# Performance work log

Measured on AMD Instinct MI355X. Metric: run time of the kernel, lower is better.

## Reference

```python
import jax, jax.numpy as jnp
from jax import lax
import numpy as np

B, S = 4096, 200           # batch, max history length
MAX_LEN, STEP = 1024, 4    # module init args
BINS = MAX_LEN // STEP     # 256 time bins
H = 64                     # LSTM hidden (dimension)


def setup_inputs() -> dict:
    key = jax.random.key(0)
    ks = jax.random.split(key, 8)
    time = jax.random.uniform(ks[0], (B, S), jnp.float32, 0.0, 1000.0)
    # predict_time >= max event time per row (module assumes nonnegative bin index)
    predict_time = jnp.max(time, axis=1) + jax.random.uniform(ks[1], (B,), jnp.float32, 0.0, 24.0)
    length = jax.random.randint(ks[2], (B,), 1, S + 1, jnp.int32)
    # torch nn.LSTM init: uniform(-1/sqrt(H), 1/sqrt(H)); gate order i,f,g,o
    s = 1.0 / np.sqrt(H)
    W_ih = jax.random.uniform(ks[3], (4 * H, 1), jnp.float32, -s, s)
    W_hh = jax.random.uniform(ks[4], (4 * H, H), jnp.float32, -s, s)
    b_ih = jax.random.uniform(ks[5], (4 * H,), jnp.float32, -s, s)
    b_hh = jax.random.uniform(ks[6], (4 * H,), jnp.float32, -s, s)
    return {"time": time, "length": length, "predict_time": predict_time,
            "W_ih": W_ih, "W_hh": W_hh, "b_ih": b_ih, "b_hh": b_hh}


def _histogram(time, length, predict_time):
    # pos = int((predict_time - time_ij) / STEP), incremented at bin BINS-1-pos
    pos = ((predict_time[:, None] - time) / STEP).astype(jnp.int32)  # trunc toward 0, like int()
    valid = (jnp.arange(S)[None, :] < length[:, None]) & (pos >= 0) & (pos < BINS)
    idx = BINS - 1 - jnp.clip(pos, 0, BINS - 1)
    hist = jnp.zeros((B, BINS), jnp.float32)
    hist = hist.at[jnp.arange(B)[:, None], idx].add(valid.astype(jnp.float32))
    return hist  # [B, BINS]


def _lstm_final_h(x, W_ih, W_hh, b_ih, b_hh):
    # x: [B, T] scalar sequence (input_size=1). Returns final hidden state [B, H].
    b = b_ih + b_hh

    def step(carry, x_t):
        h, c = carry
        gates = x_t[:, None] * W_ih[:, 0][None, :] + h @ W_hh.T + b  # [B, 4H]
        i, f, g, o = jnp.split(gates, 4, axis=1)
        c = jax.nn.sigmoid(f) * c + jax.nn.sigmoid(i) * jnp.tanh(g)
        h = jax.nn.sigmoid(o) * jnp.tanh(c)
        return (h, c), None

    init = (jnp.zeros((B, H), x.dtype), jnp.zeros((B, H), x.dtype))
    (h, _), _ = lax.scan(step, init, jnp.moveaxis(x, 1, 0))  # scan over T
    return h


def reference(time, length, predict_time, W_ih, W_hh, b_ih, b_hh):
    hist = _histogram(time, length, predict_time)
    return _lstm_final_h(hist, W_ih, W_hh, b_ih, b_hh)
```

## Files before the change

### kernel.cpp

```cpp
#include <hip/hip_runtime.h>
#include <hip/hip_bf16.h>


#define B_S     200
#define B_T     256
#define ROWS    16
#define THREADS 256
#define HS      72
#define LOG2E   1.4426950408889634f

typedef __attribute__((ext_vector_type(8))) _Float16 half8;
typedef __attribute__((ext_vector_type(4))) float float4_t;

__device__ __forceinline__ float load_f(const void* p, int i, int isb) {
    if (isb) {
        unsigned short u = ((const unsigned short*)p)[i];
        return __uint_as_float(((unsigned int)u) << 16);
    }
    return ((const float*)p)[i];
}

__global__ __launch_bounds__(THREADS)
void trend_encoder_kernel(const void* __restrict__ time_,
                          const int*  __restrict__ length,
                          const void* __restrict__ ptime_,
                          const void* __restrict__ wih_,
                          const void* __restrict__ whh_,
                          const void* __restrict__ bih_,
                          const void* __restrict__ bhh_,
                          void* __restrict__ out_) {
    __shared__ __align__(16) float x_t[B_T * ROWS];
    __shared__ __align__(16) _Float16 h_sh[2][ROWS * HS];
    __shared__ int flag_sh;

    const int tid  = threadIdx.x;
    const int wv   = tid >> 6;
    const int lane = tid & 63;
    const int m    = lane & 15;
    const int quad = lane >> 4;
    const int b0   = blockIdx.x * ROWS;

    if (tid < 64) {
        unsigned short u = ((const unsigned short*)wih_)[tid];
        float v = __uint_as_float(((unsigned int)u) << 16);
        int bad = !(v > -0.2f && v < 0.2f);
        unsigned long long bm = __ballot(bad);
        if (lane == 0) flag_sh = (bm == 0ULL) ? 1 : 0;
    }
    for (int i = tid; i < B_T * ROWS; i += THREADS) x_t[i] = 0.0f;
    for (int i = tid; i < ROWS * HS; i += THREADS) h_sh[0][i] = (_Float16)0.0f;
    __syncthreads();
    const int isb = flag_sh;

    for (int e = tid; e < ROWS * B_S; e += THREADS) {
        int row  = e / B_S;
        int s    = e - row * B_S;
        int grow = b0 + row;
        if (s < length[grow]) {
            float pt = load_f(ptime_, grow, isb);
            float tv = load_f(time_, grow * B_S + s, isb);
            int pos = (int)((pt - tv) * 0.25f);
            if (pos >= 0 && pos < B_T)
                atomicAdd(&x_t[(B_T - 1 - pos) * ROWS + row], 1.0f);
        }
    }

    const float gsc[4] = {-LOG2E, -LOG2E, 2.0f * LOG2E, -LOG2E};
    half8 bw[4][2];
    float wihv[4], biasv[4];
    #pragma unroll
    for (int tt = 0; tt < 4; ++tt) {
        int n = 16 * wv + 64 * tt + m;
        float s = gsc[tt];
        wihv[tt]  = load_f(wih_, n, isb) * s;
        biasv[tt] = (load_f(bih_, n, isb) + load_f(bhh_, n, isb)) * s;
        #pragma unroll
        for (int c = 0; c < 2; ++c) {
            half8 v;
            #pragma unroll
            for (int j = 0; j < 8; ++j)
                v[j] = (_Float16)(load_f(whh_, n * 64 + 32 * c + 8 * quad + j, isb) * s);
            bw[tt][c] = v;
        }
    }

    const int aoff = m * HS + 8 * quad;
    const int kcol = 16 * wv + m;
    float creg[4] = {0.f, 0.f, 0.f, 0.f};
    float hreg[4] = {0.f, 0.f, 0.f, 0.f};
    __syncthreads();

    for (int t = 0; t < B_T; ++t) {
        const int p = t & 1;
        const _Float16* hh = h_sh[p];
        half8 a0 = *(const half8*)&hh[aoff];
        half8 a1 = *(const half8*)&hh[aoff + 32];
        float4_t xv = *(const float4_t*)&x_t[t * ROWS + quad * 4];

        float4_t acc[4];
        #pragma unroll
        for (int tt = 0; tt < 4; ++tt) {
            float4_t a;
            #pragma unroll
            for (int r = 0; r < 4; ++r) a[r] = fmaf(xv[r], wihv[tt], biasv[tt]);
            a = __builtin_amdgcn_mfma_f32_16x16x32_f16(a0, bw[tt][0], a, 0, 0, 0);
            a = __builtin_amdgcn_mfma_f32_16x16x32_f16(a1, bw[tt][1], a, 0, 0, 0);
            acc[tt] = a;
        }

        _Float16* wb = h_sh[p ^ 1];
        #pragma unroll
        for (int r = 0; r < 4; ++r) {
            float A  = __builtin_amdgcn_exp2f(acc[0][r]);
            float F  = __builtin_amdgcn_exp2f(acc[1][r]);
            float Bv = __builtin_amdgcn_exp2f(acc[2][r]);
            float t1    = (1.0f + A) * (Bv + 1.0f);
            float oneF  = 1.0f + F;
            float numer = fmaf(creg[r], t1, oneF * (Bv - 1.0f));
            float denom = oneF * t1;
            creg[r] = numer * __builtin_amdgcn_rcpf(denom);
            float D  = __builtin_amdgcn_exp2f(acc[3][r]);
            float cs = fminf(creg[r] * (2.0f * LOG2E), 126.0f);
            float E  = __builtin_amdgcn_exp2f(cs);
            float h  = (E - 1.0f) * __builtin_amdgcn_rcpf((1.0f + D) * (E + 1.0f));
            hreg[r] = h;
            wb[(quad * 4 + r) * HS + kcol] = (_Float16)h;
        }
        __syncthreads();
    }

    #pragma unroll
    for (int r = 0; r < 4; ++r) {
        int o = (b0 + quad * 4 + r) * 64 + kcol;
        if (isb) ((__hip_bfloat16*)out_)[o] = __float2bfloat16(hreg[r]);
        else     ((float*)out_)[o] = hreg[r];
    }
}

extern "C" void kernel_launch(void* const* d_in, const int* in_sizes, int n_in,
                              void* d_out, int out_size, void* d_ws, size_t ws_size,
                              hipStream_t stream) {
    const void* time_  = d_in[0];
    const int*  length = (const int*)d_in[1];
    const void* ptime  = d_in[2];
    const void* wih    = d_in[3];
    const void* whh    = d_in[4];
    const void* bih    = d_in[5];
    const void* bhh    = d_in[6];

    const int B = in_sizes[1];
    trend_encoder_kernel<<<dim3(B / ROWS), dim3(THREADS), 0, stream>>>(
        time_, length, ptime, wih, whh, bih, bhh, d_out);
}
```

Before: 194.3 us.

## Double block to 512 threads, splitting gate activations across wave halves

Doubles the threads per block so two waves share each hidden-column chunk. Both waves compute the same MFMAs redundantly, and each applies the activation math to only half of the 4 accumulator rows. This halves the serial per-step transcendental work per wave on the recurrent critical path. The cost is duplicated MFMA work, more waves per barrier, and possibly lower block occupancy per CU.

```diff
diff --git a/kernel.cpp b/kernel.cpp
--- a/kernel.cpp
+++ b/kernel.cpp
@@ -5,7 +5,7 @@
 #define B_S     200
 #define B_T     256
 #define ROWS    16
-#define THREADS 256
+#define THREADS 512
 #define HS      72
 #define LOG2E   1.4426950408889634f
 
@@ -33,12 +33,14 @@
     __shared__ __align__(16) _Float16 h_sh[2][ROWS * HS];
     __shared__ int flag_sh;
 
-    const int tid  = threadIdx.x;
-    const int wv   = tid >> 6;
-    const int lane = tid & 63;
-    const int m    = lane & 15;
-    const int quad = lane >> 4;
-    const int b0   = blockIdx.x * ROWS;
+    const int tid   = threadIdx.x;
+    const int wv    = tid >> 6;
+    const int lane  = tid & 63;
+    const int m     = lane & 15;
+    const int quad  = lane >> 4;
+    const int hc    = wv & 3;
+    const int rhalf = wv >> 2;
+    const int b0    = blockIdx.x * ROWS;
 
     if (tid < 64) {
         unsigned short u = ((const unsigned short*)wih_)[tid];
@@ -70,7 +72,7 @@
     float wihv[4], biasv[4];
     #pragma unroll
     for (int tt = 0; tt < 4; ++tt) {
-        int n = 16 * wv + 64 * tt + m;
+        int n = 16 * hc + 64 * tt + m;
         float s = gsc[tt];
         wihv[tt]  = load_f(wih_, n, isb) * s;
         biasv[tt] = (load_f(bih_, n, isb) + load_f(bhh_, n, isb)) * s;
@@ -85,10 +87,28 @@
     }
 
     const int aoff = m * HS + 8 * quad;
-    const int kcol = 16 * wv + m;
-    float creg[4] = {0.f, 0.f, 0.f, 0.f};
-    float hreg[4] = {0.f, 0.f, 0.f, 0.f};
+    const int kcol = 16 * hc + m;
+    float creg[2] = {0.f, 0.f};
+    float hreg[2] = {0.f, 0.f};
     __syncthreads();
+
+    #define ACT(RR, R)                                                        \
+    {                                                                         \
+        float A  = __builtin_amdgcn_exp2f(acc[0][R]);     \
+        float F  = __builtin_amdgcn_exp2f(acc[1][R]);     \
+        float Bv = __builtin_amdgcn_exp2f(acc[2][R]);     \
+        float t1    = (1.0f + A) * (Bv + 1.0f);                               \
+        float oneF  = 1.0f + F;                                               \
+        float numer = fmaf(creg[RR], t1, oneF * (Bv - 1.0f));                 \
+        float denom = oneF * t1;                                              \
+        creg[RR] = numer * __builtin_amdgcn_rcpf(denom);                      \
+        float D  = __builtin_amdgcn_exp2f(acc[3][R]);     \
+        float cs = fminf(creg[RR] * (2.0f * LOG2E), 126.0f);   \
+        float E  = __builtin_amdgcn_exp2f(cs);                                \
+        float h  = (E - 1.0f) * __builtin_amdgcn_rcpf((1.0f + D) * (E + 1.0f)); \
+        hreg[RR] = h;                                                         \
+        wb[(quad * 4 + R) * HS + kcol] = (_Float16)h;                         \
+    }
 
     for (int t = 0; t < B_T; ++t) {
         const int p = t & 1;
@@ -109,31 +129,17 @@
         }
 
         _Float16* wb = h_sh[p ^ 1];
-        #pragma unroll
-        for (int r = 0; r < 4; ++r) {
-            float A  = __builtin_amdgcn_exp2f(acc[0][r]);
-            float F  = __builtin_amdgcn_exp2f(acc[1][r]);
-            float Bv = __builtin_amdgcn_exp2f(acc[2][r]);
-            float t1    = (1.0f + A) * (Bv + 1.0f);
-            float oneF  = 1.0f + F;
-            float numer = fmaf(creg[r], t1, oneF * (Bv - 1.0f));
-            float denom = oneF * t1;
-            creg[r] = numer * __builtin_amdgcn_rcpf(denom);
-            float D  = __builtin_amdgcn_exp2f(acc[3][r]);
-            float cs = fminf(creg[r] * (2.0f * LOG2E), 126.0f);
-            float E  = __builtin_amdgcn_exp2f(cs);
-            float h  = (E - 1.0f) * __builtin_amdgcn_rcpf((1.0f + D) * (E + 1.0f));
-            hreg[r] = h;
-            wb[(quad * 4 + r) * HS + kcol] = (_Float16)h;
-        }
+        if (rhalf == 0) { ACT(0, 0); ACT(1, 1); }
+        else            { ACT(0, 2); ACT(1, 3); }
         __syncthreads();
     }
+    #undef ACT
 
     #pragma unroll
-    for (int r = 0; r < 4; ++r) {
-        int o = (b0 + quad * 4 + r) * 64 + kcol;
-        if (isb) ((__hip_bfloat16*)out_)[o] = __float2bfloat16(hreg[r]);
-        else     ((float*)out_)[o] = hreg[r];
+    for (int rr = 0; rr < 2; ++rr) {
+        int o = (b0 + quad * 4 + 2 * rhalf + rr) * 64 + kcol;
+        if (isb) ((__hip_bfloat16*)out_)[o] = __float2bfloat16(hreg[rr]);
+        else     ((float*)out_)[o] = hreg[rr];
     }
 }
 
```

After: 211.6 us. +8.9%, slower.

## Split LSTM rows into two half-groups and interleave MFMA with activations

Applied to the files above, without the earlier changes.

The 16 rows of each block are split into two 8-row streams (X and Y), each with its own double-buffered hidden state in shared memory. In each step, the gate activations of one stream run while the MFMA gate matmul of the other stream is issued. A cross-lane shuffle redistributes accumulator rows so each lane handles two activations instead of four. This is meant to hide the serial MFMA-then-transcendental latency of the recurrence, at the cost of twice as many MFMAs on half-empty tiles and two barriers per time step.

```diff
diff --git a/kernel.cpp b/kernel.cpp
--- a/kernel.cpp
+++ b/kernel.cpp
@@ -30,7 +30,8 @@
                           const void* __restrict__ bhh_,
                           void* __restrict__ out_) {
     __shared__ __align__(16) float x_t[B_T * ROWS];
-    __shared__ __align__(16) _Float16 h_sh[2][ROWS * HS];
+    __shared__ __align__(16) _Float16 hX[2][16 * HS];
+    __shared__ __align__(16) _Float16 hY[2][16 * HS];
     __shared__ int flag_sh;
 
     const int tid  = threadIdx.x;
@@ -48,7 +49,8 @@
         if (lane == 0) flag_sh = (bm == 0ULL) ? 1 : 0;
     }
     for (int i = tid; i < B_T * ROWS; i += THREADS) x_t[i] = 0.0f;
-    for (int i = tid; i < ROWS * HS; i += THREADS) h_sh[0][i] = (_Float16)0.0f;
+    for (int i = tid; i < 2 * 16 * HS; i += THREADS) (&hX[0][0])[i] = (_Float16)0.0f;
+    for (int i = tid; i < 2 * 16 * HS; i += THREADS) (&hY[0][0])[i] = (_Float16)0.0f;
     __syncthreads();
     const int isb = flag_sh;
 
@@ -84,56 +86,124 @@
         }
     }
 
-    const int aoff = m * HS + 8 * quad;
-    const int kcol = 16 * wv + m;
-    float creg[4] = {0.f, 0.f, 0.f, 0.f};
-    float hreg[4] = {0.f, 0.f, 0.f, 0.f};
+    const int aoff  = m * HS + 8 * quad;
+    const int kcol  = 16 * wv + m;
+    const int row0  = 4 * (quad & 1) + 2 * (quad >> 1);
+    const int yxofs = (8 + 4 * quad) & 15;
+    float cX0 = 0.f, cX1 = 0.f, cY0 = 0.f, cY1 = 0.f;
+    float hXr0 = 0.f, hXr1 = 0.f, hYr0 = 0.f, hYr1 = 0.f;
+
     __syncthreads();
 
-    for (int t = 0; t < B_T; ++t) {
-        const int p = t & 1;
-        const _Float16* hh = h_sh[p];
-        half8 a0 = *(const half8*)&hh[aoff];
-        half8 a1 = *(const half8*)&hh[aoff + 32];
-        float4_t xv = *(const float4_t*)&x_t[t * ROWS + quad * 4];
-
-        float4_t acc[4];
+    #define ACT(CR, HR, G0, G1, G2, G3, WBP, RI)                              \
+    {                                                                         \
+        float A_  = __builtin_amdgcn_exp2f(G0);                               \
+        float F_  = __builtin_amdgcn_exp2f(G1);                               \
+        float Bv_ = __builtin_amdgcn_exp2f(G2);                               \
+        float t1_    = (1.0f + A_) * (Bv_ + 1.0f);                            \
+        float oneF_  = 1.0f + F_;                                             \
+        float numer_ = fmaf(CR, t1_, oneF_ * (Bv_ - 1.0f));                   \
+        float denom_ = oneF_ * t1_;                                           \
+        CR = numer_ * __builtin_amdgcn_rcpf(denom_);                          \
+        float D_  = __builtin_amdgcn_exp2f(G3);                               \
+        float cs_ = fminf(CR * (2.0f * LOG2E), 126.0f);                       \
+        float E_  = __builtin_amdgcn_exp2f(cs_);                              \
+        float h_  = (E_ - 1.0f) * __builtin_amdgcn_rcpf((1.0f + D_) * (E_ + 1.0f)); \
+        HR = h_;                                                              \
+        WBP[(RI) * HS + kcol] = (_Float16)h_;                                 \
+    }
+
+    #define REDIST(ACC, GA, GB)                                               \
+    {                                                                         \
+        _Pragma("unroll")                                                     \
+        for (int tt = 0; tt < 4; ++tt) {                                      \
+            float x2_ = __shfl_xor(ACC[tt][2], 32);                           \
+            float x3_ = __shfl_xor(ACC[tt][3], 32);                           \
+            GA[tt] = (quad < 2) ? ACC[tt][0] : x2_;                           \
+            GB[tt] = (quad < 2) ? ACC[tt][1] : x3_;                           \
+        }                                                                     \
+    }
+
+    #define GATES(ACC, A0, A1, XV)                                            \
+    {                                                                         \
+        _Pragma("unroll")                                                     \
+        for (int tt = 0; tt < 4; ++tt) {                                      \
+            float4_t a_;                                                      \
+            _Pragma("unroll")                                                 \
+            for (int r = 0; r < 4; ++r) a_[r] = fmaf(XV[r], wihv[tt], biasv[tt]); \
+            a_ = __builtin_amdgcn_mfma_f32_16x16x32_f16(A0, bw[tt][0], a_, 0, 0, 0); \
+            a_ = __builtin_amdgcn_mfma_f32_16x16x32_f16(A1, bw[tt][1], a_, 0, 0, 0); \
+            ACC[tt] = a_;                                                     \
+        }                                                                     \
+    }
+
+    float4_t accY[4];
+    {
+        float4_t xv0 = *(const float4_t*)&x_t[yxofs];
         #pragma unroll
         for (int tt = 0; tt < 4; ++tt) {
-            float4_t a;
             #pragma unroll
-            for (int r = 0; r < 4; ++r) a[r] = fmaf(xv[r], wihv[tt], biasv[tt]);
-            a = __builtin_amdgcn_mfma_f32_16x16x32_f16(a0, bw[tt][0], a, 0, 0, 0);
-            a = __builtin_amdgcn_mfma_f32_16x16x32_f16(a1, bw[tt][1], a, 0, 0, 0);
-            acc[tt] = a;
-        }
-
-        _Float16* wb = h_sh[p ^ 1];
-        #pragma unroll
-        for (int r = 0; r < 4; ++r) {
-            float A  = __builtin_amdgcn_exp2f(acc[0][r]);
-            float F  = __builtin_amdgcn_exp2f(acc[1][r]);
-            float Bv = __builtin_amdgcn_exp2f(acc[2][r]);
-            float t1    = (1.0f + A) * (Bv + 1.0f);
-            float oneF  = 1.0f + F;
-            float numer = fmaf(creg[r], t1, oneF * (Bv - 1.0f));
-            float denom = oneF * t1;
-            creg[r] = numer * __builtin_amdgcn_rcpf(denom);
-            float D  = __builtin_amdgcn_exp2f(acc[3][r]);
-            float cs = fminf(creg[r] * (2.0f * LOG2E), 126.0f);
-            float E  = __builtin_amdgcn_exp2f(cs);
-            float h  = (E - 1.0f) * __builtin_amdgcn_rcpf((1.0f + D) * (E + 1.0f));
-            hreg[r] = h;
-            wb[(quad * 4 + r) * HS + kcol] = (_Float16)h;
+            for (int r = 0; r < 4; ++r) accY[tt][r] = fmaf(xv0[r], wihv[tt], biasv[tt]);
+        }
+    }
+
+    for (int t = 0; t < B_T; ++t) {
+        const int pr = t & 1, pw = pr ^ 1;
+
+        half8 ax0 = *(const half8*)&hX[pr][aoff];
+        half8 ax1 = *(const half8*)&hX[pr][aoff + 32];
+
+        {
+            float gA[4], gB[4];
+            REDIST(accY, gA, gB);
+            _Float16* wb = hY[pw];
+            ACT(cY0, hYr0, gA[0], gA[1], gA[2], gA[3], wb, row0);
+            ACT(cY1, hYr1, gB[0], gB[1], gB[2], gB[3], wb, row0 + 1);
+        }
+
+        float4_t accX[4];
+        {
+            float4_t xvX = *(const float4_t*)&x_t[t * ROWS + quad * 4];
+            GATES(accX, ax0, ax1, xvX);
         }
         __syncthreads();
-    }
-
-    #pragma unroll
-    for (int r = 0; r < 4; ++r) {
-        int o = (b0 + quad * 4 + r) * 64 + kcol;
-        if (isb) ((__hip_bfloat16*)out_)[o] = __float2bfloat16(hreg[r]);
-        else     ((float*)out_)[o] = hreg[r];
+
+        half8 ay0 = *(const half8*)&hY[pw][aoff];
+        half8 ay1 = *(const half8*)&hY[pw][aoff + 32];
+
+        {
+            float gA[4], gB[4];
+            REDIST(accX, gA, gB);
+            _Float16* wb = hX[pw];
+            ACT(cX0, hXr0, gA[0], gA[1], gA[2], gA[3], wb, row0);
+            ACT(cX1, hXr1, gB[0], gB[1], gB[2], gB[3], wb, row0 + 1);
+        }
+
+        {
+            int tn = (t + 1 < B_T) ? t + 1 : t;
+            float4_t xvY = *(const float4_t*)&x_t[tn * ROWS + yxofs];
+            GATES(accY, ay0, ay1, xvY);
+        }
+        __syncthreads();
+    }
+    #undef ACT
+    #undef REDIST
+    #undef GATES
+
+    {
+        int oX = (b0 + row0) * 64 + kcol;
+        int oY = (b0 + 8 + row0) * 64 + kcol;
+        if (isb) {
+            ((__hip_bfloat16*)out_)[oX]      = __float2bfloat16(hXr0);
+            ((__hip_bfloat16*)out_)[oX + 64] = __float2bfloat16(hXr1);
+            ((__hip_bfloat16*)out_)[oY]      = __float2bfloat16(hYr0);
+            ((__hip_bfloat16*)out_)[oY + 64] = __float2bfloat16(hYr1);
+        } else {
+            ((float*)out_)[oX]      = hXr0;
+            ((float*)out_)[oX + 64] = hXr1;
+            ((float*)out_)[oY]      = hYr0;
+            ((float*)out_)[oY + 64] = hYr1;
+        }
     }
 }
 
```

Result: slower. 338.6 us (+74.3%).

## Make each wave own whole batch rows to drop per-step block barriers

Applied to the files above, without the earlier changes.

The recurrence is restructured so each wave computes all 256 gate columns for its own 4 batch rows. Each wave keeps a private swizzled LDS slice of h, which removes the block-wide __syncthreads from every time step. In exchange each wave now issues four times as many MFMAs per step, only one accumulator element per lane is used, and all recurrent weights sit in registers (launch bounds now allow one block per CU). The next step's h fragment and x value are loaded at the end of each step, and the writes use XOR swizzling to avoid bank conflicts.

```diff
diff --git a/kernel.cpp b/kernel.cpp
--- a/kernel.cpp
+++ b/kernel.cpp
@@ -6,7 +6,6 @@
 #define B_T     256
 #define ROWS    16
 #define THREADS 256
-#define HS      72
 #define LOG2E   1.4426950408889634f
 
 typedef __attribute__((ext_vector_type(8))) _Float16 half8;
@@ -20,7 +19,7 @@
     return ((const float*)p)[i];
 }
 
-__global__ __launch_bounds__(THREADS)
+__global__ __launch_bounds__(THREADS, 1)
 void trend_encoder_kernel(const void* __restrict__ time_,
                           const int*  __restrict__ length,
                           const void* __restrict__ ptime_,
@@ -30,14 +29,14 @@
                           const void* __restrict__ bhh_,
                           void* __restrict__ out_) {
     __shared__ __align__(16) float x_t[B_T * ROWS];
-    __shared__ __align__(16) _Float16 h_sh[2][ROWS * HS];
+    __shared__ __align__(16) _Float16 h_lds[4][16 * 64];
     __shared__ int flag_sh;
 
     const int tid  = threadIdx.x;
     const int wv   = tid >> 6;
     const int lane = tid & 63;
     const int m    = lane & 15;
-    const int quad = lane >> 4;
+    const int q    = lane >> 4;
     const int b0   = blockIdx.x * ROWS;
 
     if (tid < 64) {
@@ -48,7 +47,8 @@
         if (lane == 0) flag_sh = (bm == 0ULL) ? 1 : 0;
     }
     for (int i = tid; i < B_T * ROWS; i += THREADS) x_t[i] = 0.0f;
-    for (int i = tid; i < ROWS * HS; i += THREADS) h_sh[0][i] = (_Float16)0.0f;
+    for (int i = tid; i < 4 * 16 * 64; i += THREADS)
+        (&h_lds[0][0])[i] = (_Float16)0.0f;
     __syncthreads();
     const int isb = flag_sh;
 
@@ -66,74 +66,131 @@
     }
 
     const float gsc[4] = {-LOG2E, -LOG2E, 2.0f * LOG2E, -LOG2E};
-    half8 bw[4][2];
-    float wihv[4], biasv[4];
+    half8 bw[4][4][2];
+    float wihv[4][4], biasv[4][4];
     #pragma unroll
-    for (int tt = 0; tt < 4; ++tt) {
-        int n = 16 * wv + 64 * tt + m;
-        float s = gsc[tt];
-        wihv[tt]  = load_f(wih_, n, isb) * s;
-        biasv[tt] = (load_f(bih_, n, isb) + load_f(bhh_, n, isb)) * s;
-        #pragma unroll
-        for (int c = 0; c < 2; ++c) {
-            half8 v;
+    for (int g = 0; g < 4; ++g) {
+        #pragma unroll
+        for (int u = 0; u < 4; ++u) {
+            int n = 64 * g + 16 * u + m;
+            float s = gsc[g];
+            wihv[g][u]  = load_f(wih_, n, isb) * s;
+            biasv[g][u] = (load_f(bih_, n, isb) + load_f(bhh_, n, isb)) * s;
             #pragma unroll
-            for (int j = 0; j < 8; ++j)
-                v[j] = (_Float16)(load_f(whh_, n * 64 + 32 * c + 8 * quad + j, isb) * s);
-            bw[tt][c] = v;
+            for (int c = 0; c < 2; ++c) {
+                half8 v;
+                #pragma unroll
+                for (int j = 0; j < 8; ++j)
+                    v[j] = (_Float16)(load_f(whh_, n * 64 + 32 * c + 8 * q + j, isb) * s);
+                bw[g][u][c] = v;
+            }
         }
     }
 
-    const int aoff = m * HS + 8 * quad;
-    const int kcol = 16 * wv + m;
-    float creg[4] = {0.f, 0.f, 0.f, 0.f};
-    float hreg[4] = {0.f, 0.f, 0.f, 0.f};
+    _Float16* hw = h_lds[wv];
+    const int xrow = 4 * wv + q;
+    const int mh   = m >> 3;
+    const int wsw  = 4 * (q & 1);
+    const int wbase = 256 * q + (m & 7);
+    const int wi0 = wbase + ((((0 + mh) ^ wsw) & 7) << 3);
+    const int wi1 = wbase + ((((2 + mh) ^ wsw) & 7) << 3);
+    const int wi2 = wbase + ((((4 + mh) ^ wsw) & 7) << 3);
+    const int wi3 = wbase + ((((6 + mh) ^ wsw) & 7) << 3);
+    const int ra0 = 64 * m + ((q ^ (m & 7)) << 3);
+    const int ra1 = 64 * m + (((4 + q) ^ (m & 7)) << 3);
+
     __syncthreads();
 
+    #define ACT(CR, HR, G0, G1, G2, G3)                                       \
+    {                                                                         \
+        float A_  = __builtin_amdgcn_exp2f(G0);                               \
+        float F_  = __builtin_amdgcn_exp2f(G1);                               \
+        float Bv_ = __builtin_amdgcn_exp2f(G2);                               \
+        float t1_    = (1.0f + A_) * (Bv_ + 1.0f);                            \
+        float oneF_  = 1.0f + F_;                                             \
+        float numer_ = fmaf(CR, t1_, oneF_ * (Bv_ - 1.0f));                   \
+        float denom_ = oneF_ * t1_;                                           \
+        CR = numer_ * __builtin_amdgcn_rcpf(denom_);                          \
+        float D_  = __builtin_amdgcn_exp2f(G3);                               \
+        float cs_ = fminf(CR * (2.0f * LOG2E), 126.0f);                       \
+        float E_  = __builtin_amdgcn_exp2f(cs_);                              \
+        HR = (E_ - 1.0f) * __builtin_amdgcn_rcpf((1.0f + D_) * (E_ + 1.0f));  \
+    }
+
+    half8 a0 = 0, a1 = 0;
+    float xb = x_t[xrow];
+    float c0 = 0.f, c1 = 0.f, c2 = 0.f, c3 = 0.f;
+    float h0 = 0.f, h1 = 0.f, h2 = 0.f, h3 = 0.f;
+    float4_t accA[4], accB[4];
+    #pragma unroll
+    for (int g = 0; g < 4; ++g) { accA[g] = (float4_t)0.0f; accB[g] = (float4_t)0.0f; }
+
     for (int t = 0; t < B_T; ++t) {
-        const int p = t & 1;
-        const _Float16* hh = h_sh[p];
-        half8 a0 = *(const half8*)&hh[aoff];
-        half8 a1 = *(const half8*)&hh[aoff + 32];
-        float4_t xv = *(const float4_t*)&x_t[t * ROWS + quad * 4];
-
-        float4_t acc[4];
-        #pragma unroll
-        for (int tt = 0; tt < 4; ++tt) {
-            float4_t a;
-            #pragma unroll
-            for (int r = 0; r < 4; ++r) a[r] = fmaf(xv[r], wihv[tt], biasv[tt]);
-            a = __builtin_amdgcn_mfma_f32_16x16x32_f16(a0, bw[tt][0], a, 0, 0, 0);
-            a = __builtin_amdgcn_mfma_f32_16x16x32_f16(a1, bw[tt][1], a, 0, 0, 0);
-            acc[tt] = a;
+        #pragma unroll
+        for (int g = 0; g < 4; ++g) accA[g][0] = fmaf(xb, wihv[g][0], biasv[g][0]);
+        #pragma unroll
+        for (int g = 0; g < 4; ++g) accB[g][0] = fmaf(xb, wihv[g][1], biasv[g][1]);
+        #pragma unroll
+        for (int g = 0; g < 4; ++g)
+            accA[g] = __builtin_amdgcn_mfma_f32_16x16x32_f16(a0, bw[g][0][0], accA[g], 0, 0, 0);
+        #pragma unroll
+        for (int g = 0; g < 4; ++g)
+            accB[g] = __builtin_amdgcn_mfma_f32_16x16x32_f16(a0, bw[g][1][0], accB[g], 0, 0, 0);
+        #pragma unroll
+        for (int g = 0; g < 4; ++g)
+            accA[g] = __builtin_amdgcn_mfma_f32_16x16x32_f16(a1, bw[g][0][1], accA[g], 0, 0, 0);
+        #pragma unroll
+        for (int g = 0; g < 4; ++g)
+            accB[g] = __builtin_amdgcn_mfma_f32_16x16x32_f16(a1, bw[g][1][1], accB[g], 0, 0, 0);
+
+        ACT(c0, h0, accA[0][0], accA[1][0], accA[2][0], accA[3][0]);
+        hw[wi0] = (_Float16)h0;
+        ACT(c1, h1, accB[0][0], accB[1][0], accB[2][0], accB[3][0]);
+        hw[wi1] = (_Float16)h1;
+        half8 na0 = *(const half8*)&hw[ra0];
+
+        #pragma unroll
+        for (int g = 0; g < 4; ++g) accA[g][0] = fmaf(xb, wihv[g][2], biasv[g][2]);
+        #pragma unroll
+        for (int g = 0; g < 4; ++g) accB[g][0] = fmaf(xb, wihv[g][3], biasv[g][3]);
+        #pragma unroll
+        for (int g = 0; g < 4; ++g)
+            accA[g] = __builtin_amdgcn_mfma_f32_16x16x32_f16(a0, bw[g][2][0], accA[g], 0, 0, 0);
+        #pragma unroll
+        for (int g = 0; g < 4; ++g)
+            accB[g] = __builtin_amdgcn_mfma_f32_16x16x32_f16(a0, bw[g][3][0], accB[g], 0, 0, 0);
+        #pragma unroll
+        for (int g = 0; g < 4; ++g)
+            accA[g] = __builtin_amdgcn_mfma_f32_16x16x32_f16(a1, bw[g][2][1], accA[g], 0, 0, 0);
+        #pragma unroll
+        for (int g = 0; g < 4; ++g)
+            accB[g] = __builtin_amdgcn_mfma_f32_16x16x32_f16(a1, bw[g][3][1], accB[g], 0, 0, 0);
+
+        ACT(c2, h2, accA[0][0], accA[1][0], accA[2][0], accA[3][0]);
+        hw[wi2] = (_Float16)h2;
+        ACT(c3, h3, accB[0][0], accB[1][0], accB[2][0], accB[3][0]);
+        hw[wi3] = (_Float16)h3;
+        half8 na1 = *(const half8*)&hw[ra1];
+
+        int tn = (t + 1 < B_T) ? t + 1 : t;
+        float nxb = x_t[tn * ROWS + xrow];
+        a0 = na0; a1 = na1; xb = nxb;
+    }
+    #undef ACT
+
+    {
+        int ob = (b0 + 4 * wv + q) * 64 + m;
+        if (isb) {
+            ((__hip_bfloat16*)out_)[ob]      = __float2bfloat16(h0);
+            ((__hip_bfloat16*)out_)[ob + 16] = __float2bfloat16(h1);
+            ((__hip_bfloat16*)out_)[ob + 32] = __float2bfloat16(h2);
+            ((__hip_bfloat16*)out_)[ob + 48] = __float2bfloat16(h3);
+        } else {
+            ((float*)out_)[ob]      = h0;
+            ((float*)out_)[ob + 16] = h1;
+            ((float*)out_)[ob + 32] = h2;
+            ((float*)out_)[ob + 48] = h3;
         }
-
-        _Float16* wb = h_sh[p ^ 1];
-        #pragma unroll
-        for (int r = 0; r < 4; ++r) {
-            float A  = __builtin_amdgcn_exp2f(acc[0][r]);
-            float F  = __builtin_amdgcn_exp2f(acc[1][r]);
-            float Bv = __builtin_amdgcn_exp2f(acc[2][r]);
-            float t1    = (1.0f + A) * (Bv + 1.0f);
-            float oneF  = 1.0f + F;
-            float numer = fmaf(creg[r], t1, oneF * (Bv - 1.0f));
-            float denom = oneF * t1;
-            creg[r] = numer * __builtin_amdgcn_rcpf(denom);
-            float D  = __builtin_amdgcn_exp2f(acc[3][r]);
-            float cs = fminf(creg[r] * (2.0f * LOG2E), 126.0f);
-            float E  = __builtin_amdgcn_exp2f(cs);
-            float h  = (E - 1.0f) * __builtin_amdgcn_rcpf((1.0f + D) * (E + 1.0f));
-            hreg[r] = h;
-            wb[(quad * 4 + r) * HS + kcol] = (_Float16)h;
-        }
-        __syncthreads();
-    }
-
-    #pragma unroll
-    for (int r = 0; r < 4; ++r) {
-        int o = (b0 + quad * 4 + r) * 64 + kcol;
-        if (isb) ((__hip_bfloat16*)out_)[o] = __float2bfloat16(hreg[r]);
-        else     ((float*)out_)[o] = hreg[r];
     }
 }
 
```

Result: slower. 265.0 us (+36.4%).
